# Kernel tuning notes

Measured on AMD Instinct MI355X. Metric: run time of the kernel, lower is better.

The kernel has to match this reference:

```python
import jax, jax.numpy as jnp
import numpy as np

NUM_REL = 7
EPS = 1e-5
N, E = 30000, 480000
D_IN, D_H = 21, 512


def _bn(x, g, b):
    # BatchNorm1d over nodes (training-mode batch statistics, biased var like torch)
    mu = x.mean(axis=0)
    var = x.var(axis=0)
    return (x - mu) * jax.lax.rsqrt(var + EPS) * g + b


def _conv(x, src, seg_idx, lin_w, lin_b, self_w, self_b, bn_g, bn_b):
    # GeometricRelationalGraphConv: gather src features, scatter-add per (dst, relation)
    d = x.shape[1]
    msg = x[src]                                                   # (E, d)
    upd = jax.ops.segment_sum(msg, seg_idx, num_segments=N * NUM_REL)
    upd = upd.reshape(N, NUM_REL * d)                              # (N, 7*d)
    out = upd @ lin_w.T + lin_b + x @ self_w.T + self_b            # linear + self-loop
    out = _bn(out, bn_g, bn_b)                                     # conv-internal BN
    return jax.nn.relu(out)


def setup_inputs() -> dict:
    key = jax.random.key(0)
    ks = jax.random.split(key, 16)
    inp = {
        "x": jax.random.normal(ks[0], (N, D_IN), dtype=jnp.float32),
        "src": jax.random.randint(ks[1], (E,), 0, N, dtype=jnp.int32),
        "dst": jax.random.randint(ks[2], (E,), 0, N, dtype=jnp.int32),
        "rel": jax.random.randint(ks[3], (E,), 0, NUM_REL, dtype=jnp.int32),
    }
    dims = [(D_IN, D_H), (D_H, D_H), (D_H, D_H)]
    k = 4
    for i, (din, dout) in enumerate(dims):
        inp[f"lin_w{i}"] = jax.random.normal(ks[k], (dout, NUM_REL * din), dtype=jnp.float32) * 0.05
        inp[f"self_w{i}"] = jax.random.normal(ks[k + 1], (dout, din), dtype=jnp.float32) * 0.05
        k += 2
        inp[f"lin_b{i}"] = jnp.zeros((dout,), jnp.float32)
        inp[f"self_b{i}"] = jnp.zeros((dout,), jnp.float32)
        inp[f"bn1_g{i}"] = jnp.ones((dout,), jnp.float32)
        inp[f"bn1_b{i}"] = jnp.zeros((dout,), jnp.float32)
        inp[f"bn2_g{i}"] = jnp.ones((dout,), jnp.float32)
        inp[f"bn2_b{i}"] = jnp.zeros((dout,), jnp.float32)
    return inp


def reference(x, src, dst, rel,
              lin_w0, lin_b0, self_w0, self_b0, bn1_g0, bn1_b0, bn2_g0, bn2_b0,
              lin_w1, lin_b1, self_w1, self_b1, bn1_g1, bn1_b1, bn2_g1, bn2_b1,
              lin_w2, lin_b2, self_w2, self_b2, bn1_g2, bn1_b2, bn2_g2, bn2_b2):
    seg_idx = dst * NUM_REL + rel                                  # (E,)
    layers = [
        (lin_w0, lin_b0, self_w0, self_b0, bn1_g0, bn1_b0, bn2_g0, bn2_b0),
        (lin_w1, lin_b1, self_w1, self_b1, bn1_g1, bn1_b1, bn2_g1, bn2_b1),
        (lin_w2, lin_b2, self_w2, self_b2, bn1_g2, bn1_b2, bn2_g2, bn2_b2),
    ]
    hiddens = []
    h = x
    for lw, lb, sw, sb, g1, b1, g2, b2 in layers:
        h = _conv(h, src, seg_idx, lw, lb, sw, sb, g1, b1)
        h = _bn(h, g2, b2)                                         # GearNet outer BN
        hiddens.append(h)
    return jnp.concatenate(hiddens, axis=-1)                      # (N, 3*512) concat_hidden
```

## Files before the change

### kernel.cpp

```cpp
#include <hip/hip_runtime.h>

#define NN   30000
#define NE   480000
#define NR   7
#define NSEG (NN*NR)
#define DH   512
#define DIN  21
#define EPSB 1e-5f
#define KSEG 3584

typedef __attribute__((ext_vector_type(8))) short bf16x8;
typedef __attribute__((ext_vector_type(8))) unsigned short u16x8;
typedef __attribute__((ext_vector_type(4))) float f32x4;
typedef unsigned short ushortT;

static inline size_t align256(size_t x){ return (x + 255) & ~(size_t)255; }

__device__ inline float bf2f(ushortT u){
    unsigned int i = ((unsigned int)u) << 16; float f; __builtin_memcpy(&f, &i, 4); return f;
}
__device__ inline ushortT f2bf(float f){
    unsigned int i; __builtin_memcpy(&i, &f, 4);
    unsigned int r = i + 0x7FFFu + ((i >> 16) & 1u);
    return (ushortT)(r >> 16);
}

__device__ inline void load_lds16(const ushortT* g, ushortT* l){
    __builtin_amdgcn_global_load_lds((const __attribute__((address_space(1))) unsigned int*)g,
                                     (__attribute__((address_space(3))) unsigned int*)l,
                                     16, 0, 0);
}


__global__ void hist_k(const int* __restrict__ dst, const int* __restrict__ rel,
                       int* __restrict__ counts){
    int e = blockIdx.x*256 + threadIdx.x;
    if (e < NE) atomicAdd(&counts[dst[e]*NR + rel[e]], 1);
}

__global__ void scan1_k(const int* __restrict__ counts, int* __restrict__ bsum){
    __shared__ int sd[256];
    int t = threadIdx.x;
    int base = blockIdx.x*1024 + t*4;
    int s = 0;
#pragma unroll
    for (int i = 0; i < 4; i++){ int idx = base + i; if (idx < NSEG) s += counts[idx]; }
    sd[t] = s; __syncthreads();
    for (int off = 128; off > 0; off >>= 1){
        if (t < off) sd[t] += sd[t+off];
        __syncthreads();
    }
    if (t == 0) bsum[blockIdx.x] = sd[0];
}

__global__ void scan2_k(int* __restrict__ bsum, int nb, int* __restrict__ seg_start){
    __shared__ int sd[256];
    int t = threadIdx.x;
    int v = (t < nb) ? bsum[t] : 0;
    sd[t] = v; __syncthreads();
    for (int off = 1; off < 256; off <<= 1){
        int x = sd[t];
        if (t >= off) x += sd[t-off];
        __syncthreads();
        sd[t] = x; __syncthreads();
    }
    if (t < nb) bsum[t] = (t == 0) ? 0 : sd[t-1];
    if (t == 0) seg_start[NSEG] = NE;
}

__global__ void scan3_k(const int* __restrict__ counts, const int* __restrict__ bsum,
                        int* __restrict__ seg_start){
    __shared__ int sd[256];
    int t = threadIdx.x;
    int base = blockIdx.x*1024 + t*4;
    int v[4]; int s = 0;
#pragma unroll
    for (int i = 0; i < 4; i++){ int idx = base + i; v[i] = (idx < NSEG) ? counts[idx] : 0; s += v[i]; }
    sd[t] = s; __syncthreads();
    for (int off = 1; off < 256; off <<= 1){
        int x = sd[t];
        if (t >= off) x += sd[t-off];
        __syncthreads();
        sd[t] = x; __syncthreads();
    }
    int excl = sd[t] - s + bsum[blockIdx.x];
#pragma unroll
    for (int i = 0; i < 4; i++){
        int idx = base + i;
        if (idx < NSEG){ seg_start[idx] = excl; excl += v[i]; }
    }
}

__global__ void scatter_k(const int* __restrict__ src, const int* __restrict__ dst,
                          const int* __restrict__ rel, const int* __restrict__ seg_start,
                          int* __restrict__ cursor, int* __restrict__ src_sorted){
    int e = blockIdx.x*256 + threadIdx.x;
    if (e < NE){
        int s = dst[e]*NR + rel[e];
        int pos = seg_start[s] + atomicAdd(&cursor[s], 1);
        src_sorted[pos] = src[e];
    }
}


__global__ void segsum21b_k(const float* __restrict__ x0,
                            const int* __restrict__ seg_start, const int* __restrict__ src_sorted,
                            ushortT* __restrict__ Acat0){
    int n = blockIdx.x;
    int t = threadIdx.x;
    ushortT* arow = Acat0 + (long)n*256;
    if (t < DIN){
        int sb = n*NR;
        int e0 = seg_start[sb];
#pragma unroll
        for (int r = 0; r < NR; r++){
            int e1 = seg_start[sb + r + 1];
            float a = 0.f;
            for (int e = e0; e < e1; e++) a += x0[(long)src_sorted[e]*DIN + t];
            e0 = e1;
            arow[r*DIN + t] = f2bf(a);
        }
        arow[7*DIN + t] = f2bf(x0[(long)n*DIN + t]);
    }
    if (t >= 40) arow[168 + (t - 40)] = 0;
    arow[192 + t] = 0;
}


__device__ inline void segsum_body(const ushortT* __restrict__ hbf,
                                   const int* __restrict__ seg_start,
                                   const int* __restrict__ src_sorted,
                                   ushortT* __restrict__ Acat,
                                   int wid, int c0, int lane){
    const int n = c0 + wid;
    const int co = lane*8;

    int sb[8];
#pragma unroll
    for (int i = 0; i < 8; i++) sb[i] = seg_start[n*NR + i];

    ushortT* arow = Acat + (long)wid*KSEG + co;
#pragma unroll
    for (int r = 0; r < NR; r++){
        float a[8];
#pragma unroll
        for (int j = 0; j < 8; j++) a[j] = 0.f;
        int e = sb[r], e1 = sb[r+1];
        for (; e + 3 < e1; e += 4){
            u16x8 v0 = *reinterpret_cast<const u16x8*>(hbf + (long)src_sorted[e  ]*DH + co);
            u16x8 v1 = *reinterpret_cast<const u16x8*>(hbf + (long)src_sorted[e+1]*DH + co);
            u16x8 v2 = *reinterpret_cast<const u16x8*>(hbf + (long)src_sorted[e+2]*DH + co);
            u16x8 v3 = *reinterpret_cast<const u16x8*>(hbf + (long)src_sorted[e+3]*DH + co);
#pragma unroll
            for (int j = 0; j < 8; j++)
                a[j] += (bf2f((ushortT)v0[j]) + bf2f((ushortT)v1[j]))
                      + (bf2f((ushortT)v2[j]) + bf2f((ushortT)v3[j]));
        }
        for (; e < e1; e++){
            u16x8 v = *reinterpret_cast<const u16x8*>(hbf + (long)src_sorted[e]*DH + co);
#pragma unroll
            for (int j = 0; j < 8; j++) a[j] += bf2f((ushortT)v[j]);
        }
        u16x8 o;
#pragma unroll
        for (int j = 0; j < 8; j++) o[j] = f2bf(a[j]);
        *reinterpret_cast<u16x8*>(arow + r*DH) = o;
    }
}

__global__ __launch_bounds__(256)
void segsum_wave_k(const ushortT* __restrict__ hbf,
                   const int* __restrict__ seg_start, const int* __restrict__ src_sorted,
                   ushortT* __restrict__ Acat, int c0, int cn){
    const int lane = threadIdx.x & 63;
    const int gwave = (blockIdx.x*256 + threadIdx.x) >> 6;
    const int nwaves = (gridDim.x*256) >> 6;
    for (int wid = gwave; wid < cn; wid += nwaves)
        segsum_body(hbf, seg_start, src_sorted, Acat, wid, c0, lane);
}


__global__ void convw_k(const float* __restrict__ lw, const float* __restrict__ sw,
                        int d, int Kp, ushortT* __restrict__ Wc){
    int i = blockIdx.x*256 + threadIdx.x;
    if (i < DH*Kp){
        int n = i / Kp, k = i % Kp;
        float v;
        if (k < 7*d)      v = lw[(long)n*7*d + k];
        else if (k < 8*d) v = sw[(long)n*d + (k - 7*d)];
        else              v = 0.f;
        Wc[i] = f2bf(v);
    }
}


__global__ __launch_bounds__(512, 2)
void gemm8_k(const ushortT* __restrict__ A, int lda, int ntA,
             const ushortT* __restrict__ hbase, int M,
             const ushortT* __restrict__ W, int ldw,
             const float* __restrict__ b1, const float* __restrict__ b2,
             float* __restrict__ C, int ldc, int nt, float* __restrict__ sums){
    __shared__ ushortT As[2*2*64*64];
    __shared__ ushortT Bs[2*2*128*64];
    const int t = threadIdx.x;

    const int nwg = gridDim.x;
    int qq = nwg >> 3, rr = nwg & 7;
    int xcd = blockIdx.x & 7, slot = blockIdx.x >> 3;
    int l = xcd*qq + min(xcd, rr) + slot;
    const int bm = (l >> 1)*128;
    const int bn = (l & 1)*256;

    const int ur  = t >> 3;
    const int sw  = ((t & 7) ^ (ur & 7))*8;
    const int ur1 = 64 + ur;
    const int sw1 = ((t & 7) ^ (ur1 & 7))*8;
    const int arh0 = min(bm + ur, M-1);
    const int arh1 = min(bm + 64 + ur, M-1);
    const int brA0 = bn + ur,        brA1 = bn + ur1;
    const int brB0 = bn + 128 + ur,  brB1 = bn + 128 + ur1;

    auto stageA = [&](int kt, int h, int buf){
        ushortT* d = &As[(buf*2 + h)*4096];
        int row = h ? arh1 : arh0;
        const ushortT* p;
        if (kt < ntA) p = A + (long)row*lda + kt*64 + sw;
        else          p = hbase + (long)row*DH + (kt - ntA)*64 + sw;
        load_lds16(p, d + t*8);
    };
    auto stageB = [&](int kt, int h, int buf){
        ushortT* d = &Bs[(buf*2 + h)*8192];
        int r0 = h ? brB0 : brA0, r1 = h ? brB1 : brA1;
        load_lds16(W + (long)r0*ldw + kt*64 + sw,  d + t*8);
        load_lds16(W + (long)r1*ldw + kt*64 + sw1, d + (t + 512)*8);
    };

    const int w = t >> 6, lane = t & 63;
    const int wm = w >> 2, wn = w & 3;
    const int r = lane & 15, hi = lane >> 4;
    const int swzk0 = ((hi)     ^ (r & 7))*8;
    const int swzk1 = ((4 + hi) ^ (r & 7))*8;
    const int aBase = wm*4096 + r*64;
    const int bBase = (wn >> 1)*8192 + ((wn & 1)*64 + r)*64;

    f32x4 acc[4][4];
#pragma unroll
    for (int m = 0; m < 4; m++)
#pragma unroll
        for (int n = 0; n < 4; n++) acc[m][n] = (f32x4){0.f,0.f,0.f,0.f};

    stageA(0, 0, 0); stageA(0, 1, 0);
    stageB(0, 0, 0); stageB(0, 1, 0);
    stageA(1, 0, 1); stageA(1, 1, 1);
    asm volatile("s_waitcnt vmcnt(2)" ::: "memory");
    __builtin_amdgcn_s_barrier();

    for (int it = 0; it < nt; it += 2){
#pragma unroll
        for (int b = 0; b < 2; ++b){
            bf16x8 aK0[4], aK1[4];
            const int bufoA = b*8192;
            const int bufoB = b*16384;
#pragma unroll
            for (int qp = 0; qp < 4; ++qp){
                const int np = qp >> 1;
                const int swzk = (qp & 1) ? swzk1 : swzk0;
                bf16x8 bb0 = *reinterpret_cast<const bf16x8*>(&Bs[bufoB + bBase + (np*2+0)*1024 + swzk]);
                bf16x8 bb1 = *reinterpret_cast<const bf16x8*>(&Bs[bufoB + bBase + (np*2+1)*1024 + swzk]);
                if (qp == 0){
#pragma unroll
                    for (int m = 0; m < 4; m++)
                        aK0[m] = *reinterpret_cast<const bf16x8*>(&As[bufoA + aBase + m*1024 + swzk0]);
                }
                if (qp == 1){
#pragma unroll
                    for (int m = 0; m < 4; m++)
                        aK1[m] = *reinterpret_cast<const bf16x8*>(&As[bufoA + aBase + m*1024 + swzk1]);
                }
                {
                    const int ph = b*4 + qp;
                    if (ph == 0)      stageB(min(it+1, nt-1), 0, 1);
                    else if (ph == 1) stageB(min(it+1, nt-1), 1, 1);
                    else if (ph == 2) stageA(min(it+2, nt-1), 0, 0);
                    else if (ph == 3) stageA(min(it+2, nt-1), 1, 0);
                    else if (ph == 4) stageB(min(it+2, nt-1), 0, 0);
                    else if (ph == 5) stageB(min(it+2, nt-1), 1, 0);
                    else if (ph == 6) stageA(min(it+3, nt-1), 0, 1);
                    else              stageA(min(it+3, nt-1), 1, 1);
                }
                __builtin_amdgcn_s_barrier();
                asm volatile("s_waitcnt lgkmcnt(0)" ::: "memory");
                __builtin_amdgcn_sched_barrier(0);
                __builtin_amdgcn_s_setprio(1);
#pragma unroll
                for (int m = 0; m < 4; m++){
                    const bf16x8 am = (qp & 1) ? aK1[m] : aK0[m];
                    acc[m][np*2+0] = __builtin_amdgcn_mfma_f32_16x16x32_bf16(am, bb0, acc[m][np*2+0], 0, 0, 0);
                    acc[m][np*2+1] = __builtin_amdgcn_mfma_f32_16x16x32_bf16(am, bb1, acc[m][np*2+1], 0, 0, 0);
                }
                __builtin_amdgcn_s_setprio(0);
                if (qp == 3) asm volatile("s_waitcnt vmcnt(2)" ::: "memory");
                __builtin_amdgcn_s_barrier();
            }
        }
    }
    asm volatile("s_waitcnt vmcnt(0)" ::: "memory");

#pragma unroll
    for (int n = 0; n < 4; n++){
        int col = bn + wn*64 + n*16 + r;
        float bb = b1[col] + b2[col];
        float s = 0.f, s2 = 0.f;
#pragma unroll
        for (int m = 0; m < 4; m++){
            int row = bm + wm*64 + m*16 + hi*4;
#pragma unroll
            for (int j2 = 0; j2 < 4; j2++){
                if (row + j2 < M){
                    float v = acc[m][n][j2] + bb;
                    C[(long)(row + j2)*ldc + col] = v;
                    s += v; s2 = fmaf(v, v, s2);
                }
            }
        }
        s  += __shfl_xor(s, 16);  s  += __shfl_xor(s, 32);
        s2 += __shfl_xor(s2, 16); s2 += __shfl_xor(s2, 32);
        if (hi == 0){
            atomicAdd(&sums[col], s);
            atomicAdd(&sums[DH + col], s2);
        }
    }
}


__global__ void finalize_k(const float* __restrict__ sums, const float* __restrict__ g,
                           const float* __restrict__ b, float* __restrict__ ac){
    int c = blockIdx.x*256 + threadIdx.x;
    if (c < DH){
        float mu  = sums[c] * (1.f/NN);
        float var = sums[DH + c] * (1.f/NN) - mu*mu;
        var = fmaxf(var, 0.f);
        float a = g[c] * rsqrtf(var + EPSB);
        ac[c]      = a;
        ac[DH + c] = fmaf(-mu, a, b[c]);
    }
}

__global__ void bnrelu_k(float* __restrict__ o, int M, const float* __restrict__ ac,
                         float* __restrict__ sums2){
    int col = blockIdx.x*256 + threadIdx.x;
    int r0 = blockIdx.y*128;
    int r1 = min(r0 + 128, M);
    float a = ac[col], c = ac[DH + col];
    float s = 0.f, s2 = 0.f;
    for (int r = r0; r < r1; r++){
        long idx = (long)r*(3*DH) + col;
        float y = fmaxf(fmaf(a, o[idx], c), 0.f);
        o[idx] = y;
        s += y; s2 = fmaf(y, y, s2);
    }
    atomicAdd(&sums2[col], s);
    atomicAdd(&sums2[DH + col], s2);
}

__global__ void bn2write_k(float* __restrict__ o, const float* __restrict__ ac,
                           ushortT* __restrict__ hbf){
    long i = (long)blockIdx.x*256 + threadIdx.x;
    if (i < (long)NN*DH){
        int r = (int)(i >> 9);
        int c = (int)(i & 511);
        long idx = (long)r*(3*DH) + c;
        float h = fmaf(ac[c], o[idx], ac[DH + c]);
        o[idx] = h;
        hbf[i] = f2bf(h);
    }
}


extern "C" void kernel_launch(void* const* d_in, const int* in_sizes, int n_in,
                              void* d_out, int out_size, void* d_ws, size_t ws_size,
                              hipStream_t stream){
    const float* x0  = (const float*)d_in[0];
    const int*   src = (const int*)d_in[1];
    const int*   dst = (const int*)d_in[2];
    const int*   rel = (const int*)d_in[3];
    const float* lin_w[3]  = {(const float*)d_in[4],  (const float*)d_in[12], (const float*)d_in[20]};
    const float* self_w[3] = {(const float*)d_in[5],  (const float*)d_in[13], (const float*)d_in[21]};
    const float* lin_b[3]  = {(const float*)d_in[6],  (const float*)d_in[14], (const float*)d_in[22]};
    const float* self_b[3] = {(const float*)d_in[7],  (const float*)d_in[15], (const float*)d_in[23]};
    const float* bn1_g[3]  = {(const float*)d_in[8],  (const float*)d_in[16], (const float*)d_in[24]};
    const float* bn1_b[3]  = {(const float*)d_in[9],  (const float*)d_in[17], (const float*)d_in[25]};
    const float* bn2_g[3]  = {(const float*)d_in[10], (const float*)d_in[18], (const float*)d_in[26]};
    const float* bn2_b[3]  = {(const float*)d_in[11], (const float*)d_in[19], (const float*)d_in[27]};

    char* ws = (char*)d_ws;
    size_t off = 0;
    auto alloc = [&](size_t bytes)->char*{ char* p = ws + off; off = align256(off + bytes); return p; };

    int*     seg_start  = (int*)alloc((size_t)(NSEG+1)*4);
    int*     bsum       = (int*)alloc(1024*4);
    int*     src_sorted = (int*)alloc((size_t)NE*4);
    float*   stats      = (float*)alloc((size_t)8*DH*4);
    float*   sums1 = stats;            float* sums2 = stats + 2*DH;
    float*   ac1   = stats + 4*DH;     float* ac2   = stats + 6*DH;
    ushortT* hbf    = (ushortT*)alloc((size_t)NN*DH*2);
    ushortT* Wcat   = (ushortT*)alloc((size_t)DH*4096*2);

    size_t remain = (ws_size > off) ? (ws_size - off) : 0;
    ushortT* Acat   = (ushortT*)(ws + off);
    int*     counts = (int*)Acat;
    int*     cursor = counts + NSEG;
    ushortT* Acat0  = (ushortT*)align256((size_t)(cursor + NSEG));

    long max_nodes = (long)(remain / ((size_t)KSEG*2));
    int chunk;
    if (max_nodes >= NN) chunk = NN;
    else { chunk = (int)(max_nodes & ~255L); if (chunk < 2560) chunk = 2560; }

    hipMemsetAsync(counts, 0, (size_t)NSEG*4, stream);
    hipMemsetAsync(cursor, 0, (size_t)NSEG*4, stream);
    hist_k<<<(NE+255)/256, 256, 0, stream>>>(dst, rel, counts);
    int nb = (NSEG + 1023)/1024;
    scan1_k<<<nb, 256, 0, stream>>>(counts, bsum);
    scan2_k<<<1, 256, 0, stream>>>(bsum, nb, seg_start);
    scan3_k<<<nb, 256, 0, stream>>>(counts, bsum, seg_start);
    scatter_k<<<(NE+255)/256, 256, 0, stream>>>(src, dst, rel, seg_start, cursor, src_sorted);

    float* dout = (float*)d_out;

    for (int layer = 0; layer < 3; layer++){
        int d  = (layer == 0) ? DIN : DH;
        int Kp = (layer == 0) ? 256 : 4096;
        convw_k<<<(DH*Kp + 255)/256, 256, 0, stream>>>(lin_w[layer], self_w[layer], d, Kp, Wcat);
        hipMemsetAsync(stats, 0, (size_t)4*DH*4, stream);

        if (layer == 0){
            segsum21b_k<<<NN, 64, 0, stream>>>(x0, seg_start, src_sorted, Acat0);
            gemm8_k<<<((NN + 127)/128)*2, 512, 0, stream>>>(
                Acat0, 256, 4, Acat0, NN, Wcat, 256,
                lin_b[layer], self_b[layer],
                dout + layer*DH, 3*DH, 4, sums1);
        } else {
            for (int c0 = 0; c0 < NN; c0 += chunk){
                int cn = (NN - c0 < chunk) ? (NN - c0) : chunk;
                int sgrid = (cn + 3)/4; if (sgrid > 2048) sgrid = 2048;
                segsum_wave_k<<<sgrid, 256, 0, stream>>>(
                    hbf, seg_start, src_sorted, Acat, c0, cn);
                gemm8_k<<<((cn + 127)/128)*2, 512, 0, stream>>>(
                    Acat, KSEG, 56, hbf + (long)c0*DH, cn, Wcat, 4096,
                    lin_b[layer], self_b[layer],
                    dout + (long)c0*(3*DH) + layer*DH, 3*DH, 64, sums1);
            }
        }

        finalize_k<<<2, 256, 0, stream>>>(sums1, bn1_g[layer], bn1_b[layer], ac1);
        bnrelu_k<<<dim3(2, (NN+127)/128), 256, 0, stream>>>(dout + layer*DH, NN, ac1, sums2);
        finalize_k<<<2, 256, 0, stream>>>(sums2, bn2_g[layer], bn2_b[layer], ac2);
        bn2write_k<<<((long)NN*DH + 255)/256, 256, 0, stream>>>(dout + layer*DH, ac2, hbf);
    }
}
```

Before: 992.7 us.

## Restructure GEMM mainloop to triple-buffered A with one barrier per k-tile

Replaces the 8-phase interleaved staging loop, which had two barriers per quarter-step, with a simpler per-k-tile loop. A is triple-buffered and prefetched two tiles ahead, B is double-buffered and prefetched one ahead, and each iteration issues 32 MFMAs followed by a single barrier. The aim is to cut barrier and synchronisation overhead in the main GEMM. In exchange it uses more LDS, which may affect occupancy at 2 blocks per CU, and it loads all fragments up front, which may raise register pressure and give less fine-grained overlap.

```diff
diff --git a/kernel.cpp b/kernel.cpp
--- a/kernel.cpp
+++ b/kernel.cpp
@@ -195,12 +195,12 @@
 
 
 __global__ __launch_bounds__(512, 2)
-void gemm8_k(const ushortT* __restrict__ A, int lda, int ntA,
+void gemm3_k(const ushortT* __restrict__ A, int lda, int ntA,
              const ushortT* __restrict__ hbase, int M,
              const ushortT* __restrict__ W, int ldw,
              const float* __restrict__ b1, const float* __restrict__ b2,
              float* __restrict__ C, int ldc, int nt, float* __restrict__ sums){
-    __shared__ ushortT As[2*2*64*64];
+    __shared__ ushortT As[3*2*64*64];
     __shared__ ushortT Bs[2*2*128*64];
     const int t = threadIdx.x;
 
@@ -220,19 +220,27 @@
     const int brA0 = bn + ur,        brA1 = bn + ur1;
     const int brB0 = bn + 128 + ur,  brB1 = bn + 128 + ur1;
 
-    auto stageA = [&](int kt, int h, int buf){
-        ushortT* d = &As[(buf*2 + h)*4096];
-        int row = h ? arh1 : arh0;
-        const ushortT* p;
-        if (kt < ntA) p = A + (long)row*lda + kt*64 + sw;
-        else          p = hbase + (long)row*DH + (kt - ntA)*64 + sw;
-        load_lds16(p, d + t*8);
+    auto stageA = [&](int kt, int buf){
+        ushortT* d = &As[buf*8192];
+        const ushortT* p0;
+        const ushortT* p1;
+        if (kt < ntA){
+            p0 = A + (long)arh0*lda + kt*64 + sw;
+            p1 = A + (long)arh1*lda + kt*64 + sw;
+        } else {
+            int k0 = (kt - ntA)*64;
+            p0 = hbase + (long)arh0*DH + k0 + sw;
+            p1 = hbase + (long)arh1*DH + k0 + sw;
+        }
+        load_lds16(p0, d + t*8);
+        load_lds16(p1, d + 4096 + t*8);
     };
-    auto stageB = [&](int kt, int h, int buf){
-        ushortT* d = &Bs[(buf*2 + h)*8192];
-        int r0 = h ? brB0 : brA0, r1 = h ? brB1 : brA1;
-        load_lds16(W + (long)r0*ldw + kt*64 + sw,  d + t*8);
-        load_lds16(W + (long)r1*ldw + kt*64 + sw1, d + (t + 512)*8);
+    auto stageB = [&](int kt, int buf){
+        ushortT* d = &Bs[buf*16384];
+        load_lds16(W + (long)brA0*ldw + kt*64 + sw,  d + t*8);
+        load_lds16(W + (long)brA1*ldw + kt*64 + sw1, d + (t + 512)*8);
+        load_lds16(W + (long)brB0*ldw + kt*64 + sw,  d + 8192 + t*8);
+        load_lds16(W + (long)brB1*ldw + kt*64 + sw1, d + 8192 + (t + 512)*8);
     };
 
     const int w = t >> 6, lane = t & 63;
@@ -249,62 +257,52 @@
 #pragma unroll
         for (int n = 0; n < 4; n++) acc[m][n] = (f32x4){0.f,0.f,0.f,0.f};
 
-    stageA(0, 0, 0); stageA(0, 1, 0);
-    stageB(0, 0, 0); stageB(0, 1, 0);
-    stageA(1, 0, 1); stageA(1, 1, 1);
+    stageA(0, 0);
+    stageB(0, 0);
+    if (nt > 1) stageA(1, 1);
     asm volatile("s_waitcnt vmcnt(2)" ::: "memory");
     __builtin_amdgcn_s_barrier();
 
-    for (int it = 0; it < nt; it += 2){
-#pragma unroll
-        for (int b = 0; b < 2; ++b){
-            bf16x8 aK0[4], aK1[4];
-            const int bufoA = b*8192;
-            const int bufoB = b*16384;
-#pragma unroll
-            for (int qp = 0; qp < 4; ++qp){
-                const int np = qp >> 1;
-                const int swzk = (qp & 1) ? swzk1 : swzk0;
-                bf16x8 bb0 = *reinterpret_cast<const bf16x8*>(&Bs[bufoB + bBase + (np*2+0)*1024 + swzk]);
-                bf16x8 bb1 = *reinterpret_cast<const bf16x8*>(&Bs[bufoB + bBase + (np*2+1)*1024 + swzk]);
-                if (qp == 0){
-#pragma unroll
-                    for (int m = 0; m < 4; m++)
-                        aK0[m] = *reinterpret_cast<const bf16x8*>(&As[bufoA + aBase + m*1024 + swzk0]);
-                }
-                if (qp == 1){
-#pragma unroll
-                    for (int m = 0; m < 4; m++)
-                        aK1[m] = *reinterpret_cast<const bf16x8*>(&As[bufoA + aBase + m*1024 + swzk1]);
-                }
-                {
-                    const int ph = b*4 + qp;
-                    if (ph == 0)      stageB(min(it+1, nt-1), 0, 1);
-                    else if (ph == 1) stageB(min(it+1, nt-1), 1, 1);
-                    else if (ph == 2) stageA(min(it+2, nt-1), 0, 0);
-                    else if (ph == 3) stageA(min(it+2, nt-1), 1, 0);
-                    else if (ph == 4) stageB(min(it+2, nt-1), 0, 0);
-                    else if (ph == 5) stageB(min(it+2, nt-1), 1, 0);
-                    else if (ph == 6) stageA(min(it+3, nt-1), 0, 1);
-                    else              stageA(min(it+3, nt-1), 1, 1);
-                }
-                __builtin_amdgcn_s_barrier();
-                asm volatile("s_waitcnt lgkmcnt(0)" ::: "memory");
-                __builtin_amdgcn_sched_barrier(0);
-                __builtin_amdgcn_s_setprio(1);
-#pragma unroll
-                for (int m = 0; m < 4; m++){
-                    const bf16x8 am = (qp & 1) ? aK1[m] : aK0[m];
-                    acc[m][np*2+0] = __builtin_amdgcn_mfma_f32_16x16x32_bf16(am, bb0, acc[m][np*2+0], 0, 0, 0);
-                    acc[m][np*2+1] = __builtin_amdgcn_mfma_f32_16x16x32_bf16(am, bb1, acc[m][np*2+1], 0, 0, 0);
-                }
-                __builtin_amdgcn_s_setprio(0);
-                if (qp == 3) asm volatile("s_waitcnt vmcnt(2)" ::: "memory");
-                __builtin_amdgcn_s_barrier();
-            }
-        }
-    }
-    asm volatile("s_waitcnt vmcnt(0)" ::: "memory");
+    for (int j = 0; j < nt; ++j){
+        const int aoff = (j % 3)*8192;
+        const int boff = (j & 1)*16384;
+
+        bf16x8 aK0[4], aK1[4], bK0[4], bK1[4];
+#pragma unroll
+        for (int m = 0; m < 4; m++){
+            aK0[m] = *reinterpret_cast<const bf16x8*>(&As[aoff + aBase + m*1024 + swzk0]);
+            aK1[m] = *reinterpret_cast<const bf16x8*>(&As[aoff + aBase + m*1024 + swzk1]);
+        }
+#pragma unroll
+        for (int n = 0; n < 4; n++){
+            bK0[n] = *reinterpret_cast<const bf16x8*>(&Bs[boff + bBase + n*1024 + swzk0]);
+            bK1[n] = *reinterpret_cast<const bf16x8*>(&Bs[boff + bBase + n*1024 + swzk1]);
+        }
+
+        const bool haveB = (j + 1 < nt);
+        const bool haveA = (j + 2 < nt);
+        if (haveB) stageB(j + 1, (j + 1) & 1);
+        if (haveA) stageA(j + 2, (j + 2) % 3);
+
+        asm volatile("s_waitcnt lgkmcnt(0)" ::: "memory");
+        __builtin_amdgcn_sched_barrier(0);
+        __builtin_amdgcn_s_setprio(1);
+#pragma unroll
+        for (int m = 0; m < 4; m++)
+#pragma unroll
+            for (int n = 0; n < 4; n++)
+                acc[m][n] = __builtin_amdgcn_mfma_f32_16x16x32_bf16(aK0[m], bK0[n], acc[m][n], 0, 0, 0);
+#pragma unroll
+        for (int m = 0; m < 4; m++)
+#pragma unroll
+            for (int n = 0; n < 4; n++)
+                acc[m][n] = __builtin_amdgcn_mfma_f32_16x16x32_bf16(aK1[m], bK1[n], acc[m][n], 0, 0, 0);
+        __builtin_amdgcn_s_setprio(0);
+
+        if (haveA) asm volatile("s_waitcnt vmcnt(2)" ::: "memory");
+        else       asm volatile("s_waitcnt vmcnt(0)" ::: "memory");
+        __builtin_amdgcn_s_barrier();
+    }
 
 #pragma unroll
     for (int n = 0; n < 4; n++){
@@ -436,7 +434,7 @@
 
         if (layer == 0){
             segsum21b_k<<<NN, 64, 0, stream>>>(x0, seg_start, src_sorted, Acat0);
-            gemm8_k<<<((NN + 127)/128)*2, 512, 0, stream>>>(
+            gemm3_k<<<((NN + 127)/128)*2, 512, 0, stream>>>(
                 Acat0, 256, 4, Acat0, NN, Wcat, 256,
                 lin_b[layer], self_b[layer],
                 dout + layer*DH, 3*DH, 4, sums1);
@@ -446,7 +444,7 @@
                 int sgrid = (cn + 3)/4; if (sgrid > 2048) sgrid = 2048;
                 segsum_wave_k<<<sgrid, 256, 0, stream>>>(
                     hbf, seg_start, src_sorted, Acat, c0, cn);
-                gemm8_k<<<((cn + 127)/128)*2, 512, 0, stream>>>(
+                gemm3_k<<<((cn + 127)/128)*2, 512, 0, stream>>>(
                     Acat, KSEG, 56, hbf + (long)c0*DH, cn, Wcat, 4096,
                     lin_b[layer], self_b[layer],
                     dout + (long)c0*(3*DH) + layer*DH, 3*DH, 64, sums1);
```

After: 951.9 us. 1.04x faster.
